# Kernel optimization log

Hardware: AMD Instinct MI355X
Metric: run time of the kernel (lower is better)

## Reference

```python
import jax, jax.numpy as jnp
import numpy as np

HIDDEN = 1024
VOCAB = 50257


def setup_inputs() -> dict:
    key = jax.random.key(0)
    ks = jax.random.split(key, 9)
    s = 0.02
    return {
        "token": jax.random.randint(ks[0], (1,), 0, VOCAB, dtype=jnp.int64),
        "hidden": jax.random.normal(ks[1], (1, 1, HIDDEN), dtype=jnp.float32),
        "emb": jax.random.normal(ks[2], (VOCAB, HIDDEN), dtype=jnp.float32) * s,
        "w_ih": jax.random.normal(ks[3], (3 * HIDDEN, HIDDEN), dtype=jnp.float32) * s,
        "w_hh": jax.random.normal(ks[4], (3 * HIDDEN, HIDDEN), dtype=jnp.float32) * s,
        "b_ih": jax.random.normal(ks[5], (3 * HIDDEN,), dtype=jnp.float32) * s,
        "b_hh": jax.random.normal(ks[6], (3 * HIDDEN,), dtype=jnp.float32) * s,
        "w_out": jax.random.normal(ks[7], (VOCAB, HIDDEN), dtype=jnp.float32) * s,
        "b_out": jax.random.normal(ks[8], (VOCAB,), dtype=jnp.float32) * s,
    }


def reference(token, hidden, emb, w_ih, w_hh, b_ih, b_hh, w_out, b_out):
    # embed + relu: [1, H]
    x = jax.nn.relu(emb[token].reshape(1, HIDDEN))
    h = hidden[0]  # [1, H]
    # single-step GRU (PyTorch gate order r, z, n; separate biases)
    gi = x @ w_ih.T + b_ih  # [1, 3H]
    gh = h @ w_hh.T + b_hh  # [1, 3H]
    i_r, i_z, i_n = jnp.split(gi, 3, axis=-1)
    h_r, h_z, h_n = jnp.split(gh, 3, axis=-1)
    r = jax.nn.sigmoid(i_r + h_r)
    z = jax.nn.sigmoid(i_z + h_z)
    n = jnp.tanh(i_n + r * h_n)
    h_new = (1.0 - z) * n + z * h  # [1, H]
    # output projection + log-softmax over vocab
    logits = h_new @ w_out.T + b_out  # [1, V]
    logp = jax.nn.log_softmax(logits, axis=1)
    return logp, h_new[None]  # ([1, V], [1, 1, H])
```

## Files before the change

kernel.cpp:

```cpp
#include <hip/hip_runtime.h>
#include <math.h>

#define HIDDEN 1024
#define VOCAB 50257
#define K2_BLOCKS 1024
#define K2_WAVES (K2_BLOCKS * 4)

__device__ __forceinline__ float wave_reduce_sum(float v) {
#pragma unroll
    for (int m = 1; m < 64; m <<= 1) v += __shfl_xor(v, m, 64);
    return v;
}

__global__ __launch_bounds__(192) void gru_kernel(
    const int* token_p, const float* __restrict__ hidden, const float* __restrict__ emb,
    const float* __restrict__ w_ih, const float* __restrict__ w_hh,
    const float* __restrict__ b_ih, const float* __restrict__ b_hh,
    float* __restrict__ h_new_out) {
    const int g = threadIdx.x >> 6;
    const int lane = threadIdx.x & 63;
    const int j = blockIdx.x;

    const int token = token_p[0];
    const float4* x4 = (const float4*)(emb + (size_t)token * HIDDEN);
    const float4* h4 = (const float4*)hidden;

    const float4* wi = (const float4*)(w_ih + (size_t)(g * HIDDEN + j) * HIDDEN);
    const float4* wh = (const float4*)(w_hh + (size_t)(g * HIDDEN + j) * HIDDEN);

    float acc_i = 0.f, acc_h = 0.f;
#pragma unroll
    for (int k = 0; k < 4; ++k) {
        const int idx = k * 64 + lane;
        float4 e = x4[idx];
        float4 h = h4[idx];
        float4 a = wi[idx];
        float4 b = wh[idx];
        e.x = fmaxf(e.x, 0.f); e.y = fmaxf(e.y, 0.f);
        e.z = fmaxf(e.z, 0.f); e.w = fmaxf(e.w, 0.f);
        acc_i += a.x * e.x + a.y * e.y + a.z * e.z + a.w * e.w;
        acc_h += b.x * h.x + b.y * h.y + b.z * h.z + b.w * h.w;
    }
    acc_i = wave_reduce_sum(acc_i);
    acc_h = wave_reduce_sum(acc_h);

    __shared__ float red_i[3], red_h[3];
    if (lane == 0) { red_i[g] = acc_i; red_h[g] = acc_h; }
    __syncthreads();

    if (threadIdx.x == 0) {
        const float i_r = red_i[0] + b_ih[j];
        const float i_z = red_i[1] + b_ih[HIDDEN + j];
        const float i_n = red_i[2] + b_ih[2 * HIDDEN + j];
        const float h_r = red_h[0] + b_hh[j];
        const float h_z = red_h[1] + b_hh[HIDDEN + j];
        const float h_n = red_h[2] + b_hh[2 * HIDDEN + j];
        const float r = 1.f / (1.f + expf(-(i_r + h_r)));
        const float z = 1.f / (1.f + expf(-(i_z + h_z)));
        const float n = tanhf(i_n + r * h_n);
        h_new_out[j] = (1.f - z) * n + z * hidden[j];
    }
}

__global__ __launch_bounds__(256) void logits_kernel(
    const float* __restrict__ h_new, const float* __restrict__ w_out,
    const float* __restrict__ b_out, float* __restrict__ logits,
    float* __restrict__ partials) {
    const int wave = threadIdx.x >> 6;
    const int lane = threadIdx.x & 63;
    const int gw = blockIdx.x * 4 + wave;

    const float4* h4 = (const float4*)h_new;
    float4 hs[4];
#pragma unroll
    for (int k = 0; k < 4; ++k) hs[k] = h4[k * 64 + lane];

    float m = -INFINITY, s = 0.f;
    for (int v = gw; v < VOCAB; v += K2_WAVES) {
        const float4* w4 = (const float4*)(w_out + (size_t)v * HIDDEN);
        float acc = 0.f;
#pragma unroll
        for (int k = 0; k < 4; ++k) {
            float4 w = w4[k * 64 + lane];
            acc += w.x * hs[k].x + w.y * hs[k].y + w.z * hs[k].z + w.w * hs[k].w;
        }
        acc = wave_reduce_sum(acc);
        const float l = acc + b_out[v];
        if (lane == 0) logits[v] = l;
        if (l > m) { s *= expf(m - l); m = l; }
        s += expf(l - m);
    }

    __shared__ float sm[4], ss[4];
    if (lane == 0) { sm[wave] = m; ss[wave] = s; }
    __syncthreads();
    if (threadIdx.x == 0) {
        float M = fmaxf(fmaxf(sm[0], sm[1]), fmaxf(sm[2], sm[3]));
        float S = ss[0] * expf(sm[0] - M) + ss[1] * expf(sm[1] - M) +
                  ss[2] * expf(sm[2] - M) + ss[3] * expf(sm[3] - M);
        partials[2 * blockIdx.x]     = M;
        partials[2 * blockIdx.x + 1] = S;
    }
}

__global__ __launch_bounds__(1024) void lse_combine_kernel(
    const float* __restrict__ partials, float* __restrict__ scalars) {
    const int t = threadIdx.x;
    __shared__ float red[1024];

    const float m = partials[2 * t];
    const float s = partials[2 * t + 1];

    red[t] = m;
    __syncthreads();
    for (int st = 512; st > 0; st >>= 1) {
        if (t < st) red[t] = fmaxf(red[t], red[t + st]);
        __syncthreads();
    }
    const float M = red[0];
    __syncthreads();

    red[t] = s * expf(m - M);
    __syncthreads();
    for (int st = 512; st > 0; st >>= 1) {
        if (t < st) red[t] += red[t + st];
        __syncthreads();
    }
    if (t == 0) scalars[0] = M + logf(red[0]);
}

__global__ __launch_bounds__(256) void logp_kernel(
    float* __restrict__ logits, const float* __restrict__ scalars) {
    const int i = blockIdx.x * blockDim.x + threadIdx.x;
    if (i < VOCAB) logits[i] -= scalars[0];
}

extern "C" void kernel_launch(void* const* d_in, const int* in_sizes, int n_in,
                              void* d_out, int out_size, void* d_ws, size_t ws_size,
                              hipStream_t stream) {
    const int*   token  = (const int*)d_in[0];
    const float* hidden = (const float*)d_in[1];
    const float* emb    = (const float*)d_in[2];
    const float* w_ih   = (const float*)d_in[3];
    const float* w_hh   = (const float*)d_in[4];
    const float* b_ih   = (const float*)d_in[5];
    const float* b_hh   = (const float*)d_in[6];
    const float* w_out  = (const float*)d_in[7];
    const float* b_out  = (const float*)d_in[8];

    float* out     = (float*)d_out;
    float* h_new   = out + VOCAB;
    float* logits  = out;
    float* ws      = (float*)d_ws;
    float* partials = ws;
    float* scalars  = ws + 2 * K2_BLOCKS;

    gru_kernel<<<HIDDEN, 192, 0, stream>>>(token, hidden, emb, w_ih, w_hh,
                                           b_ih, b_hh, h_new);
    logits_kernel<<<K2_BLOCKS, 256, 0, stream>>>(h_new, w_out, b_out, logits, partials);
    lse_combine_kernel<<<1, 1024, 0, stream>>>(partials, scalars);
    logp_kernel<<<(VOCAB + 255) / 256, 256, 0, stream>>>(logits, scalars);
}
```

Measured before the change: 46.87 us.

## Fuse LSE combine with log-prob subtract and unroll logits loop by two rows

The separate single-block LSE combine kernel and the log-prob subtract kernel become one finalize kernel. Each of its 64 blocks redundantly combines the 1024 partials using wave shuffles and then subtracts the constant from a strided slice of logits with float4 accesses. The logits loop now processes two vocab rows per iteration, giving more loads in flight per wave. h_new is also written to an aligned workspace copy because out+VOCAB is not 16-byte aligned for float4 reads. The cost is redundant reduction work in every finalize block and extra registers in the logits loop.

```diff
diff --git a/kernel.cpp b/kernel.cpp
--- a/kernel.cpp
+++ b/kernel.cpp
@@ -4,7 +4,7 @@
 #define HIDDEN 1024
 #define VOCAB 50257
 #define K2_BLOCKS 1024
-#define K2_WAVES (K2_BLOCKS * 4)
+#define NW (K2_BLOCKS * 4)
 
 __device__ __forceinline__ float wave_reduce_sum(float v) {
 #pragma unroll
@@ -16,7 +16,7 @@
     const int* token_p, const float* __restrict__ hidden, const float* __restrict__ emb,
     const float* __restrict__ w_ih, const float* __restrict__ w_hh,
     const float* __restrict__ b_ih, const float* __restrict__ b_hh,
-    float* __restrict__ h_new_out) {
+    float* __restrict__ h_new_out, float* __restrict__ h_new_ws) {
     const int g = threadIdx.x >> 6;
     const int lane = threadIdx.x & 63;
     const int j = blockIdx.x;
@@ -24,7 +24,6 @@
     const int token = token_p[0];
     const float4* x4 = (const float4*)(emb + (size_t)token * HIDDEN);
     const float4* h4 = (const float4*)hidden;
-
     const float4* wi = (const float4*)(w_ih + (size_t)(g * HIDDEN + j) * HIDDEN);
     const float4* wh = (const float4*)(w_hh + (size_t)(g * HIDDEN + j) * HIDDEN);
 
@@ -58,7 +57,9 @@
         const float r = 1.f / (1.f + expf(-(i_r + h_r)));
         const float z = 1.f / (1.f + expf(-(i_z + h_z)));
         const float n = tanhf(i_n + r * h_n);
-        h_new_out[j] = (1.f - z) * n + z * hidden[j];
+        const float hv = (1.f - z) * n + z * hidden[j];
+        h_new_out[j] = hv;
+        h_new_ws[j] = hv;
     }
 }
 
@@ -76,19 +77,34 @@
     for (int k = 0; k < 4; ++k) hs[k] = h4[k * 64 + lane];
 
     float m = -INFINITY, s = 0.f;
-    for (int v = gw; v < VOCAB; v += K2_WAVES) {
-        const float4* w4 = (const float4*)(w_out + (size_t)v * HIDDEN);
-        float acc = 0.f;
+    for (int v = gw; v < VOCAB; v += 2 * NW) {
+        const int v2 = v + NW;
+        const bool has2 = (v2 < VOCAB);
+        const float4* w1 = (const float4*)(w_out + (size_t)v * HIDDEN);
+        const float4* w2 = (const float4*)(w_out + (size_t)(has2 ? v2 : v) * HIDDEN);
+        float a1 = 0.f, a2 = 0.f;
 #pragma unroll
         for (int k = 0; k < 4; ++k) {
-            float4 w = w4[k * 64 + lane];
-            acc += w.x * hs[k].x + w.y * hs[k].y + w.z * hs[k].z + w.w * hs[k].w;
+            const int idx = k * 64 + lane;
+            float4 x = w1[idx];
+            float4 y = w2[idx];
+            a1 += x.x * hs[k].x + x.y * hs[k].y + x.z * hs[k].z + x.w * hs[k].w;
+            a2 += y.x * hs[k].x + y.y * hs[k].y + y.z * hs[k].z + y.w * hs[k].w;
         }
-        acc = wave_reduce_sum(acc);
-        const float l = acc + b_out[v];
-        if (lane == 0) logits[v] = l;
-        if (l > m) { s *= expf(m - l); m = l; }
-        s += expf(l - m);
+        a1 = wave_reduce_sum(a1);
+        a2 = wave_reduce_sum(a2);
+
+        const float l1 = a1 + b_out[v];
+        if (lane == 0) logits[v] = l1;
+        if (l1 > m) { s *= expf(m - l1); m = l1; }
+        s += expf(l1 - m);
+
+        if (has2) {
+            const float l2 = a2 + b_out[v2];
+            if (lane == 0) logits[v2] = l2;
+            if (l2 > m) { s *= expf(m - l2); m = l2; }
+            s += expf(l2 - m);
+        }
     }
 
     __shared__ float sm[4], ss[4];
@@ -98,41 +114,51 @@
         float M = fmaxf(fmaxf(sm[0], sm[1]), fmaxf(sm[2], sm[3]));
         float S = ss[0] * expf(sm[0] - M) + ss[1] * expf(sm[1] - M) +
                   ss[2] * expf(sm[2] - M) + ss[3] * expf(sm[3] - M);
-        partials[2 * blockIdx.x]     = M;
+        partials[2 * blockIdx.x] = M;
         partials[2 * blockIdx.x + 1] = S;
     }
 }
 
-__global__ __launch_bounds__(1024) void lse_combine_kernel(
-    const float* __restrict__ partials, float* __restrict__ scalars) {
+__global__ __launch_bounds__(256) void finalize_kernel(
+    const float* __restrict__ partials, float* __restrict__ logits) {
     const int t = threadIdx.x;
-    __shared__ float red[1024];
+    const int wave = t >> 6;
+    const int lane = t & 63;
 
-    const float m = partials[2 * t];
-    const float s = partials[2 * t + 1];
+    float m = -INFINITY, s = 0.f;
+#pragma unroll
+    for (int i = 0; i < K2_BLOCKS / 256; ++i) {
+        const int idx = i * 256 + t;
+        const float pm = partials[2 * idx];
+        const float ps = partials[2 * idx + 1];
+        const float M = fmaxf(m, pm);
+        s = s * expf(m - M) + ps * expf(pm - M);
+        m = M;
+    }
+#pragma unroll
+    for (int o = 1; o < 64; o <<= 1) {
+        const float pm = __shfl_xor(m, o, 64);
+        const float ps = __shfl_xor(s, o, 64);
+        const float M = fmaxf(m, pm);
+        s = s * expf(m - M) + ps * expf(pm - M);
+        m = M;
+    }
+    __shared__ float sm[4], ss[4];
+    if (lane == 0) { sm[wave] = m; ss[wave] = s; }
+    __syncthreads();
+    const float M = fmaxf(fmaxf(sm[0], sm[1]), fmaxf(sm[2], sm[3]));
+    const float S = ss[0] * expf(sm[0] - M) + ss[1] * expf(sm[1] - M) +
+                    ss[2] * expf(sm[2] - M) + ss[3] * expf(sm[3] - M);
+    const float c = M + logf(S);
 
-    red[t] = m;
-    __syncthreads();
-    for (int st = 512; st > 0; st >>= 1) {
-        if (t < st) red[t] = fmaxf(red[t], red[t + st]);
-        __syncthreads();
+    float4* l4 = (float4*)logits;
+    const int n4 = VOCAB / 4;
+    for (int i = blockIdx.x * 256 + t; i < n4; i += gridDim.x * 256) {
+        float4 x = l4[i];
+        x.x -= c; x.y -= c; x.z -= c; x.w -= c;
+        l4[i] = x;
     }
-    const float M = red[0];
-    __syncthreads();
-
-    red[t] = s * expf(m - M);
-    __syncthreads();
-    for (int st = 512; st > 0; st >>= 1) {
-        if (t < st) red[t] += red[t + st];
-        __syncthreads();
-    }
-    if (t == 0) scalars[0] = M + logf(red[0]);
-}
-
-__global__ __launch_bounds__(256) void logp_kernel(
-    float* __restrict__ logits, const float* __restrict__ scalars) {
-    const int i = blockIdx.x * blockDim.x + threadIdx.x;
-    if (i < VOCAB) logits[i] -= scalars[0];
+    if (blockIdx.x == 0 && t == 0) logits[VOCAB - 1] -= c;
 }
 
 extern "C" void kernel_launch(void* const* d_in, const int* in_sizes, int n_in,
@@ -148,16 +174,16 @@
     const float* w_out  = (const float*)d_in[7];
     const float* b_out  = (const float*)d_in[8];
 
-    float* out     = (float*)d_out;
-    float* h_new   = out + VOCAB;
-    float* logits  = out;
-    float* ws      = (float*)d_ws;
+    float* out      = (float*)d_out;
+    float* h_new    = out + VOCAB;
+    float* logits   = out;
+    float* ws       = (float*)d_ws;
     float* partials = ws;
-    float* scalars  = ws + 2 * K2_BLOCKS;
+    float* h_new_ws = ws + 2 * K2_BLOCKS;
 
     gru_kernel<<<HIDDEN, 192, 0, stream>>>(token, hidden, emb, w_ih, w_hh,
-                                           b_ih, b_hh, h_new);
-    logits_kernel<<<K2_BLOCKS, 256, 0, stream>>>(h_new, w_out, b_out, logits, partials);
-    lse_combine_kernel<<<1, 1024, 0, stream>>>(partials, scalars);
-    logp_kernel<<<(VOCAB + 255) / 256, 256, 0, stream>>>(logits, scalars);
+                                           b_ih, b_hh, h_new, h_new_ws);
+    logits_kernel<<<K2_BLOCKS, 256, 0, stream>>>(h_new_ws, w_out, b_out, logits,
+                                                 partials);
+    finalize_kernel<<<64, 256, 0, stream>>>(partials, logits);
 }
```

New measurement: 45.97 us. No clear change (-1.9%).
